# Kernel tuning notes

Measured on AMD Instinct MI355X. Metric: run time of the kernel, lower is better.

The kernel has to match this reference:

```python
import jax, jax.numpy as jnp
import numpy as np

RES = 512
RANK = 48
OUT = 32
N = 1_000_000
INIT = 0.1


def _contract_linf(xyz, aabb):
    # L-infinity cuboid contraction of unbounded coords into [-1,1]^3.
    center = (aabb[:3] + aabb[3:]) * 0.5
    half = jnp.maximum((aabb[3:] - aabb[:3]) * 0.5, 1e-6)
    x = (xyz - center) / half
    linf = jnp.max(jnp.abs(x), axis=-1, keepdims=True)
    safe = jnp.maximum(linf, 1.0)
    scale = jnp.where(linf > 1.0, (2.0 - 1.0 / safe) / safe, 1.0)
    return jnp.clip(x * scale, -1.0, 1.0)


def _sample_plane(plane, gx, gy):
    # plane: [R, Res, Res]; gx,gy in [-1,1] shape [N]; bilinear, align_corners=True.
    res = plane.shape[-1]
    fx = (gx + 1.0) * 0.5 * (res - 1)
    fy = (gy + 1.0) * 0.5 * (res - 1)
    x0 = jnp.clip(jnp.floor(fx), 0, res - 2).astype(jnp.int32)
    y0 = jnp.clip(jnp.floor(fy), 0, res - 2).astype(jnp.int32)
    wx = fx - x0
    wy = fy - y0
    x1 = x0 + 1
    y1 = y0 + 1
    # gathers -> [R, N]
    v = (plane[:, y0, x0] * ((1 - wy) * (1 - wx))
         + plane[:, y0, x1] * ((1 - wy) * wx)
         + plane[:, y1, x0] * (wy * (1 - wx))
         + plane[:, y1, x1] * (wy * wx))
    return v


def _sample_line(line, g):
    # line: [R, Res]; 1-D linear interp along the resolution axis (align_corners=True).
    res = line.shape[-1]
    f = (g + 1.0) * 0.5 * (res - 1)
    i0 = jnp.clip(jnp.floor(f), 0, res - 2).astype(jnp.int32)
    w = f - i0
    return line[:, i0] * (1 - w) + line[:, i0 + 1] * w  # [R, N]


def setup_inputs() -> dict:
    key = jax.random.key(0)
    ks = jax.random.split(key, 9)
    coordinates = jax.random.normal(ks[0], (N, 3), dtype=jnp.float32) * 1.5  # some points outside aabb
    aabb = jnp.array([-1.0, -1.0, -1.0, 1.0, 1.0, 1.0], dtype=jnp.float32)
    plane_xy = jax.random.normal(ks[1], (RANK, RES, RES), dtype=jnp.float32) * INIT
    plane_xz = jax.random.normal(ks[2], (RANK, RES, RES), dtype=jnp.float32) * INIT
    plane_yz = jax.random.normal(ks[3], (RANK, RES, RES), dtype=jnp.float32) * INIT
    line_z = jax.random.normal(ks[4], (RANK, RES), dtype=jnp.float32) * INIT
    line_y = jax.random.normal(ks[5], (RANK, RES), dtype=jnp.float32) * INIT
    line_x = jax.random.normal(ks[6], (RANK, RES), dtype=jnp.float32) * INIT
    W = jax.random.normal(ks[7], (OUT, RANK), dtype=jnp.float32) * INIT
    b = jnp.zeros((OUT,), dtype=jnp.float32)
    return {"coordinates": coordinates, "aabb": aabb,
            "plane_xy": plane_xy, "plane_xz": plane_xz, "plane_yz": plane_yz,
            "line_z": line_z, "line_y": line_y, "line_x": line_x,
            "W": W, "b": b}


def reference(coordinates, aabb, plane_xy, plane_xz, plane_yz, line_z, line_y, line_x, W, b):
    c = _contract_linf(coordinates, aabb)  # [N,3] in [-1,1]
    cx, cy, cz = c[:, 0], c[:, 1], c[:, 2]
    # VM decomposition: plane(a,b) * line(c), summed over the three permutations -> [R, N]
    vm = (_sample_plane(plane_xy, cx, cy) * _sample_line(line_z, cz)
          + _sample_plane(plane_xz, cx, cz) * _sample_line(line_y, cy)
          + _sample_plane(plane_yz, cy, cz) * _sample_line(line_x, cx))
    # projection rank -> out_channels: [N, OUT]
    return jnp.einsum('rn,or->no', vm, W) + b
```

## Files before the change

kernel.cpp:

```cpp
#include <hip/hip_runtime.h>
#include <stdint.h>

#define RES 512
#define RANK 48
#define OUT_CH 32
#define KBITS 5
#define NBKT (1 << (3 * KBITS))
#define STR 32

typedef unsigned int u32;
typedef unsigned short u16;
typedef u32 u32x4 __attribute__((ext_vector_type(4)));


static __device__ __forceinline__ u16 f2bf(float f){
  u32 u = __float_as_uint(f);
  u32 r = (u + 0x7fffu + ((u >> 16) & 1u)) >> 16;
  return (u16)r;
}

static __device__ __forceinline__ void axis_setup(float c, int& o, float& w){
  float f = (c + 1.f) * 255.5f;
  float of = fminf(fmaxf(floorf(f), 0.f), 510.f);
  o = (int)of; w = f - of;
}

static __device__ __forceinline__ void contract(const float* __restrict__ aabb,
                                                float px, float py, float pz,
                                                float& cx, float& cy, float& cz){
  float c0 = (aabb[0] + aabb[3]) * 0.5f;
  float c1 = (aabb[1] + aabb[4]) * 0.5f;
  float c2 = (aabb[2] + aabb[5]) * 0.5f;
  float h0 = fmaxf((aabb[3] - aabb[0]) * 0.5f, 1e-6f);
  float h1 = fmaxf((aabb[4] - aabb[1]) * 0.5f, 1e-6f);
  float h2 = fmaxf((aabb[5] - aabb[2]) * 0.5f, 1e-6f);
  float x0 = (px - c0) / h0;
  float x1 = (py - c1) / h1;
  float x2 = (pz - c2) / h2;
  float linf = fmaxf(fabsf(x0), fmaxf(fabsf(x1), fabsf(x2)));
  float scale = 1.f;
  if (linf > 1.f){ float inv = 1.f / linf; scale = (2.f - inv) * inv; }
  cx = fminf(fmaxf(x0 * scale, -1.f), 1.f);
  cy = fminf(fmaxf(x1 * scale, -1.f), 1.f);
  cz = fminf(fmaxf(x2 * scale, -1.f), 1.f);
}

static __device__ __forceinline__ u32 spread3(u32 x){
  x &= 0x3FF;
  x = (x | (x << 16)) & 0x030000FF;
  x = (x | (x <<  8)) & 0x0300F00F;
  x = (x | (x <<  4)) & 0x030C30C3;
  x = (x | (x <<  2)) & 0x09249249;
  return x;
}

static __device__ __forceinline__ u32 morton_key(float cx, float cy, float cz){
  u32 kx = (u32)fminf(fmaxf((cx + 1.f) * 16.f, 0.f), 31.f);
  u32 ky = (u32)fminf(fmaxf((cy + 1.f) * 16.f, 0.f), 31.f);
  u32 kz = (u32)fminf(fmaxf((cz + 1.f) * 16.f, 0.f), 31.f);
  return spread3(kx) | (spread3(ky) << 1) | (spread3(kz) << 2);
}


__global__ void zero_hist(u32* __restrict__ hist)
{
  hist[blockIdx.x * 1024 + threadIdx.x] = 0u;
}


#define TRANS_P 3072
#define TRANS_L 6

template<bool STAGE>
__global__ void prep_fused(const float* __restrict__ pxy, const float* __restrict__ pxz,
                           const float* __restrict__ pyz,
                           const float* __restrict__ lz, const float* __restrict__ ly,
                           const float* __restrict__ lx,
                           const float* __restrict__ coords, const float* __restrict__ aabb,
                           u32* __restrict__ dstP, u32* __restrict__ dstL,
                           u32* __restrict__ hist, u32* __restrict__ keyrank,
                           float4* __restrict__ staged, int n)
{
  __shared__ u32 lds[256 * 25];
  int bid = blockIdx.x;
  int tid = threadIdx.x;
  if (bid < TRANS_P){
    int xh = bid & 1, y = (bid >> 1) & 511, p = bid >> 10;
    const float* src = (p == 0) ? pxy : (p == 1) ? pxz : pyz;
    int x = xh * 256 + tid;
    #pragma unroll
    for (int r2 = 0; r2 < 24; ++r2){
      float f0 = src[((size_t)(2 * r2) * RES + y) * RES + x];
      float f1 = src[((size_t)(2 * r2 + 1) * RES + y) * RES + x];
      lds[tid * 25 + r2] = (u32)f2bf(f0) | ((u32)f2bf(f1) << 16);
    }
    __syncthreads();
    u32* dplane = dstP + (size_t)p * (RES * RES * STR);
    size_t base = ((size_t)y * RES + xh * 256) * STR;
    for (int t = tid; t < 256 * STR; t += 256){
      int tex = t >> 5, r = t & 31;
      dplane[base + t] = (r < 24) ? lds[tex * 25 + r] : 0u;
    }
  } else if (bid < TRANS_P + TRANS_L){
    int g = (bid - TRANS_P) * 256 + tid;
    if (g < 3 * RES){
      int p = g >> 9, i = g & 511;
      const float* src = (p == 0) ? lz : (p == 1) ? ly : lx;
      u32* d = dstL + (size_t)g * STR;
      #pragma unroll
      for (int r2 = 0; r2 < 24; ++r2){
        float f0 = src[(2 * r2) * RES + i];
        float f1 = src[(2 * r2 + 1) * RES + i];
        d[r2] = (u32)f2bf(f0) | ((u32)f2bf(f1) << 16);
      }
      #pragma unroll
      for (int r2 = 24; r2 < STR; ++r2) d[r2] = 0u;
    }
  } else {
    int i = (bid - TRANS_P - TRANS_L) * 256 + tid;
    if (i < n){
      float cx, cy, cz;
      contract(aabb, coords[3*i], coords[3*i+1], coords[3*i+2], cx, cy, cz);
      u32 key = morton_key(cx, cy, cz);
      u32 rank = atomicAdd(hist + key, 1u);
      keyrank[i] = (rank << 15) | key;
      if (STAGE) staged[i] = make_float4(cx, cy, cz, __uint_as_float((u32)i));
    }
  }
}


__global__ void scan_kernel(u32* __restrict__ hist)
{
  __shared__ u32 part[1024];
  int tid = threadIdx.x;
  int base = tid * 32;
  u32 loc[32];
  u32 s = 0;
  #pragma unroll
  for (int j = 0; j < 32; j++){ loc[j] = hist[base + j]; s += loc[j]; }
  part[tid] = s;
  __syncthreads();
  for (int off = 1; off < 1024; off <<= 1){
    u32 v = 0;
    if (tid >= off) v = part[tid - off];
    __syncthreads();
    part[tid] += v;
    __syncthreads();
  }
  u32 run = part[tid] - s;
  #pragma unroll
  for (int j = 0; j < 32; j++){ u32 t = loc[j]; hist[base + j] = run; run += t; }
}


__global__ void key_scatter_staged(const u32* __restrict__ base, const u32* __restrict__ keyrank,
                                   const float4* __restrict__ staged, float4* __restrict__ sorted, int n)
{
  int i = blockIdx.x * 256 + threadIdx.x;
  if (i >= n) return;
  u32 kr = keyrank[i];
  u32 pos = base[kr & 0x7FFFu] + (kr >> 15);
  sorted[pos] = staged[i];
}


__global__ void key_scatter(const float* __restrict__ coords, const float* __restrict__ aabb,
                            const u32* __restrict__ base, const u32* __restrict__ keyrank,
                            float4* __restrict__ sorted, int n)
{
  int i = blockIdx.x * 256 + threadIdx.x;
  if (i >= n) return;
  float cx, cy, cz;
  contract(aabb, coords[3*i], coords[3*i+1], coords[3*i+2], cx, cy, cz);
  u32 kr = keyrank[i];
  u32 pos = base[kr & 0x7FFFu] + (kr >> 15);
  sorted[pos] = make_float4(cx, cy, cz, __uint_as_float((u32)i));
}


#define EXLO(u) __uint_as_float((u) << 16)
#define EXHI(u) __uint_as_float((u) & 0xffff0000u)

#define CORN_INIT(ps, taddr, wc) \
  { u32x4 _t = *(const u32x4*)(taddr); \
    _Pragma("unroll") for (int c = 0; c < 4; c++){ \
      ps[2*c] = EXLO(_t[c]) * (wc); ps[2*c+1] = EXHI(_t[c]) * (wc); } }

#define CORN_ACC(ps, taddr, wc) \
  { u32x4 _t = *(const u32x4*)(taddr); \
    _Pragma("unroll") for (int c = 0; c < 4; c++){ \
      ps[2*c] = fmaf(EXLO(_t[c]), (wc), ps[2*c]); ps[2*c+1] = fmaf(EXHI(_t[c]), (wc), ps[2*c+1]); } }

template<bool SORTED>
__global__ __launch_bounds__(256, 2)
void geo_coop(const float4* __restrict__ sorted,
              const float* __restrict__ coords, const float* __restrict__ aabb,
              const u32* __restrict__ pl, const u32* __restrict__ ln,
              const float* __restrict__ W, const float* __restrict__ bias,
              float* __restrict__ out, int n, int nwg)
{
  __shared__ __align__(16) float Wlds[8 * 49 * 4];
  __shared__ __align__(16) float vmlds[32][68];

  for (int e = threadIdx.x; e < 8 * RANK * 4; e += 256){
    int k = e / (RANK * 4);
    int rem = e - k * (RANK * 4);
    int r = rem >> 2, j = rem & 3;
    Wlds[(k * 49 + r) * 4 + j] = W[(4 * k + j) * RANK + r];
  }
  __syncthreads();

  int bid = blockIdx.x;
  int swz;
  if (SORTED){
    int q = nwg >> 3, r8 = nwg & 7;
    int xcd = bid & 7, sub = bid >> 3;
    swz = (xcd < r8 ? xcd * (q + 1) : r8 * (q + 1) + (xcd - r8) * q) + sub;
  } else {
    swz = bid;
  }

  int g = threadIdx.x >> 3;
  int k = threadIdx.x & 7;
  int i = swz * 32 + g;
  bool valid = i < n;
  int ic = valid ? i : (n - 1);

  float cx, cy, cz; u32 oidx;
  if (SORTED){
    u32x4 pr = __builtin_nontemporal_load((const u32x4*)(sorted + ic));
    cx = __uint_as_float(pr[0]);
    cy = __uint_as_float(pr[1]);
    cz = __uint_as_float(pr[2]);
    oidx = pr[3];
  } else {
    contract(aabb, coords[3*ic], coords[3*ic+1], coords[3*ic+2], cx, cy, cz);
    oidx = (u32)ic;
  }

  int ox, oy, oz; float wx, wy, wz;
  axis_setup(cx, ox, wx); axis_setup(cy, oy, wy); axis_setup(cz, oz, wz);
  float uxw = 1.f - wx, uyw = 1.f - wy, uzw = 1.f - wz;

  const u32* A   = pl + ((size_t)oy * RES + ox) * STR + 4 * k;
  const u32* B   = pl + (size_t)RES * RES * STR     + ((size_t)oz * RES + ox) * STR + 4 * k;
  const u32* C   = pl + (size_t)2 * RES * RES * STR + ((size_t)oz * RES + oy) * STR + 4 * k;
  const u32* LZp = ln +                          (size_t)oz * STR + 4 * k;
  const u32* LYp = ln + (size_t)RES * STR     + (size_t)oy * STR + 4 * k;
  const u32* LXp = ln + (size_t)2 * RES * STR + (size_t)ox * STR + 4 * k;

  float vm8[8];
  #pragma unroll
  for (int j = 0; j < 8; j++) vm8[j] = 0.f;

  {
    u32x4 l0 = *(const u32x4*)(LZp);
    u32x4 l1 = *(const u32x4*)(LZp + STR);
    float lv8[8], ps8[8];
    #pragma unroll
    for (int c = 0; c < 4; c++){
      float a0 = EXLO(l0[c]), a1 = EXHI(l0[c]);
      float b0 = EXLO(l1[c]), b1 = EXHI(l1[c]);
      lv8[2*c]   = fmaf(wz, b0 - a0, a0);
      lv8[2*c+1] = fmaf(wz, b1 - a1, a1);
    }
    CORN_INIT(ps8, A,                 uyw * uxw);
    CORN_ACC (ps8, A + STR,           uyw * wx);
    CORN_ACC (ps8, A + RES * STR,     wy * uxw);
    CORN_ACC (ps8, A + RES * STR + STR, wy * wx);
    #pragma unroll
    for (int j = 0; j < 8; j++) vm8[j] = fmaf(ps8[j], lv8[j], vm8[j]);
  }
  {
    u32x4 l0 = *(const u32x4*)(LYp);
    u32x4 l1 = *(const u32x4*)(LYp + STR);
    float lv8[8], ps8[8];
    #pragma unroll
    for (int c = 0; c < 4; c++){
      float a0 = EXLO(l0[c]), a1 = EXHI(l0[c]);
      float b0 = EXLO(l1[c]), b1 = EXHI(l1[c]);
      lv8[2*c]   = fmaf(wy, b0 - a0, a0);
      lv8[2*c+1] = fmaf(wy, b1 - a1, a1);
    }
    CORN_INIT(ps8, B,                 uzw * uxw);
    CORN_ACC (ps8, B + STR,           uzw * wx);
    CORN_ACC (ps8, B + RES * STR,     wz * uxw);
    CORN_ACC (ps8, B + RES * STR + STR, wz * wx);
    #pragma unroll
    for (int j = 0; j < 8; j++) vm8[j] = fmaf(ps8[j], lv8[j], vm8[j]);
  }
  {
    u32x4 l0 = *(const u32x4*)(LXp);
    u32x4 l1 = *(const u32x4*)(LXp + STR);
    float lv8[8], ps8[8];
    #pragma unroll
    for (int c = 0; c < 4; c++){
      float a0 = EXLO(l0[c]), a1 = EXHI(l0[c]);
      float b0 = EXLO(l1[c]), b1 = EXHI(l1[c]);
      lv8[2*c]   = fmaf(wx, b0 - a0, a0);
      lv8[2*c+1] = fmaf(wx, b1 - a1, a1);
    }
    CORN_INIT(ps8, C,                 uzw * uyw);
    CORN_ACC (ps8, C + STR,           uzw * wy);
    CORN_ACC (ps8, C + RES * STR,     wz * uyw);
    CORN_ACC (ps8, C + RES * STR + STR, wz * wy);
    #pragma unroll
    for (int j = 0; j < 8; j++) vm8[j] = fmaf(ps8[j], lv8[j], vm8[j]);
  }

  *(float4*)&vmlds[g][8 * k]     = make_float4(vm8[0], vm8[1], vm8[2], vm8[3]);
  *(float4*)&vmlds[g][8 * k + 4] = make_float4(vm8[4], vm8[5], vm8[6], vm8[7]);
  __syncthreads();

  float vmv[RANK];
  #pragma unroll
  for (int qd = 0; qd < 12; qd++){
    float4 v4 = *(const float4*)&vmlds[g][qd * 4];
    vmv[4*qd+0] = v4.x; vmv[4*qd+1] = v4.y; vmv[4*qd+2] = v4.z; vmv[4*qd+3] = v4.w;
  }
  float4 accv = ((const float4*)bias)[k];
  const float4* wk = (const float4*)(Wlds + (size_t)k * 49 * 4);
  #pragma unroll
  for (int r = 0; r < RANK; r++){
    float4 w4 = wk[r];
    accv.x = fmaf(vmv[r], w4.x, accv.x);
    accv.y = fmaf(vmv[r], w4.y, accv.y);
    accv.z = fmaf(vmv[r], w4.z, accv.z);
    accv.w = fmaf(vmv[r], w4.w, accv.w);
  }

  if (valid){
    *(float4*)(out + (size_t)oidx * 32 + 4 * k) = accv;
  }
}


__global__ __launch_bounds__(256, 2)
void geo_direct(const float* __restrict__ coords, const float* __restrict__ aabb,
                const float* __restrict__ PXY, const float* __restrict__ PXZ, const float* __restrict__ PYZ,
                const float* __restrict__ LZ, const float* __restrict__ LY, const float* __restrict__ LX,
                const float* __restrict__ W, const float* __restrict__ bias,
                float* __restrict__ out, int n)
{
  __shared__ __align__(16) float Wt[RANK * OUT_CH];
  for (int t = threadIdx.x; t < RANK * OUT_CH; t += 256){
    int r = t >> 5, o = t & 31;
    Wt[t] = W[o * RANK + r];
  }
  __syncthreads();

  int i = blockIdx.x * 256 + threadIdx.x;
  if (i >= n) return;

  float cx, cy, cz;
  contract(aabb, coords[3*i], coords[3*i+1], coords[3*i+2], cx, cy, cz);
  int ox, oy, oz; float wx, wy, wz;
  axis_setup(cx, ox, wx); axis_setup(cy, oy, wy); axis_setup(cz, oz, wz);

  int offA = oy * RES + ox, offB = oz * RES + ox, offC = oz * RES + oy;
  float uxw = 1.f - wx, uyw = 1.f - wy, uzw = 1.f - wz;
  float aw00 = uyw*uxw, aw01 = uyw*wx, aw10 = wy*uxw, aw11 = wy*wx;
  float bw00 = uzw*uxw, bw01 = uzw*wx, bw10 = wz*uxw, bw11 = wz*wx;
  float cw00 = uzw*uyw, cw01 = uzw*wy, cw10 = wz*uyw, cw11 = wz*wy;

  float acc[OUT_CH];
  #pragma unroll
  for (int o = 0; o < 8; o++){
    float4 bv = *(const float4*)(bias + o * 4);
    acc[4*o+0] = bv.x; acc[4*o+1] = bv.y; acc[4*o+2] = bv.z; acc[4*o+3] = bv.w;
  }
  const float4* Wt4 = (const float4*)Wt;

  for (int r = 0; r < RANK; r++){
    const float* pA = PXY + (size_t)r * RES * RES;
    const float* pB = PXZ + (size_t)r * RES * RES;
    const float* pC = PYZ + (size_t)r * RES * RES;
    float va = fmaf(pA[offA], aw00, fmaf(pA[offA+1], aw01, fmaf(pA[offA+RES], aw10, pA[offA+RES+1]*aw11)));
    float vb = fmaf(pB[offB], bw00, fmaf(pB[offB+1], bw01, fmaf(pB[offB+RES], bw10, pB[offB+RES+1]*bw11)));
    float vc = fmaf(pC[offC], cw00, fmaf(pC[offC+1], cw01, fmaf(pC[offC+RES], cw10, pC[offC+RES+1]*cw11)));
    float l0;
    l0 = LZ[r * RES + oz];
    float lzv = fmaf(wz, LZ[r * RES + oz + 1] - l0, l0);
    l0 = LY[r * RES + oy];
    float lyv = fmaf(wy, LY[r * RES + oy + 1] - l0, l0);
    l0 = LX[r * RES + ox];
    float lxv = fmaf(wx, LX[r * RES + ox + 1] - l0, l0);
    float vm = fmaf(va, lzv, fmaf(vb, lyv, vc * lxv));
    const float4* wrow = Wt4 + r * 8;
    #pragma unroll
    for (int q = 0; q < 8; q++){
      float4 w4 = wrow[q];
      acc[4*q+0] = fmaf(vm, w4.x, acc[4*q+0]); acc[4*q+1] = fmaf(vm, w4.y, acc[4*q+1]);
      acc[4*q+2] = fmaf(vm, w4.z, acc[4*q+2]); acc[4*q+3] = fmaf(vm, w4.w, acc[4*q+3]);
    }
  }

  float4* o4 = (float4*)(out + (size_t)i * 32);
  #pragma unroll
  for (int q = 0; q < 8; q++)
    o4[q] = make_float4(acc[4*q+0], acc[4*q+1], acc[4*q+2], acc[4*q+3]);
}


extern "C" void kernel_launch(void* const* d_in, const int* in_sizes, int n_in,
                              void* d_out, int out_size, void* d_ws, size_t ws_size,
                              hipStream_t stream)
{
  const float* coords = (const float*)d_in[0];
  const float* aabb   = (const float*)d_in[1];
  const float* pxy    = (const float*)d_in[2];
  const float* pxz    = (const float*)d_in[3];
  const float* pyz    = (const float*)d_in[4];
  const float* lz     = (const float*)d_in[5];
  const float* ly     = (const float*)d_in[6];
  const float* lx     = (const float*)d_in[7];
  const float* W      = (const float*)d_in[8];
  const float* bias   = (const float*)d_in[9];
  float* out = (float*)d_out;
  int n = in_sizes[0] / 3;
  int nwg256 = (n + 255) / 256;
  int nwg32  = (n + 31) / 32;

  const size_t planesU = (size_t)3 * RES * RES * STR;
  const size_t linesU  = (size_t)3 * RES * STR;
  const size_t histU   = NBKT;
  const size_t keyrU   = (size_t)n;
  const size_t sortedU = (size_t)4 * n;
  const size_t stagedU = (size_t)4 * n;
  const size_t needStaged = (planesU + linesU + histU + keyrU + sortedU + stagedU) * 4;
  const size_t needFull   = (planesU + linesU + histU + keyrU + sortedU) * 4;

  if (ws_size >= needStaged){
    u32* pl      = (u32*)d_ws;
    u32* ln      = pl + planesU;
    u32* hist    = ln + linesU;
    u32* keyrank = hist + histU;
    float4* sorted = (float4*)(keyrank + keyrU);
    float4* staged = sorted + n;
    zero_hist<<<NBKT / 1024, 1024, 0, stream>>>(hist);
    prep_fused<true><<<TRANS_P + TRANS_L + nwg256, 256, 0, stream>>>(
        pxy, pxz, pyz, lz, ly, lx, coords, aabb, pl, ln, hist, keyrank, staged, n);
    scan_kernel<<<1, 1024, 0, stream>>>(hist);
    key_scatter_staged<<<nwg256, 256, 0, stream>>>(hist, keyrank, staged, sorted, n);
    geo_coop<true><<<nwg32, 256, 0, stream>>>(sorted, nullptr, nullptr, pl, ln, W, bias, out, n, nwg32);
  } else if (ws_size >= needFull){
    u32* pl      = (u32*)d_ws;
    u32* ln      = pl + planesU;
    u32* hist    = ln + linesU;
    u32* keyrank = hist + histU;
    float4* sorted = (float4*)(keyrank + keyrU);
    zero_hist<<<NBKT / 1024, 1024, 0, stream>>>(hist);
    prep_fused<false><<<TRANS_P + TRANS_L + nwg256, 256, 0, stream>>>(
        pxy, pxz, pyz, lz, ly, lx, coords, aabb, pl, ln, hist, keyrank, nullptr, n);
    scan_kernel<<<1, 1024, 0, stream>>>(hist);
    key_scatter<<<nwg256, 256, 0, stream>>>(coords, aabb, hist, keyrank, sorted, n);
    geo_coop<true><<<nwg32, 256, 0, stream>>>(sorted, nullptr, nullptr, pl, ln, W, bias, out, n, nwg32);
  } else if (ws_size >= (planesU + linesU) * 4){
    u32* pl = (u32*)d_ws;
    u32* ln = pl + planesU;
    prep_fused<false><<<TRANS_P + TRANS_L, 256, 0, stream>>>(
        pxy, pxz, pyz, lz, ly, lx, coords, aabb, pl, ln, (u32*)pl, (u32*)pl, nullptr, 0);
    geo_coop<false><<<nwg32, 256, 0, stream>>>(nullptr, coords, aabb, pl, ln, W, bias, out, n, nwg32);
  } else {
    geo_direct<<<nwg256, 256, 0, stream>>>(coords, aabb, pxy, pxz, pyz, lz, ly, lx, W, bias, out, n);
  }
}
```

Before: 340.3 us.

## Split histogram scan across blocks and raise geo_coop occupancy hint

Replaces the single-block 32K-bucket exclusive scan with a two-level scan: 32 blocks each scan 1024 buckets and write block totals, then a tiny kernel scans the totals, and the scatter kernels add the block offset. This spreads the scan over many CUs instead of one workgroup, at the cost of an extra launch and an extra lookup per point in the scatter. It also raises the geo_coop launch_bounds minimum blocks per CU from 2 to 8, which can force register spilling in the main gather kernel.

```diff
diff --git a/kernel.cpp b/kernel.cpp
--- a/kernel.cpp
+++ b/kernel.cpp
@@ -130,51 +130,59 @@
 }
 
 
-__global__ void scan_kernel(u32* __restrict__ hist)
+__global__ void scan_blocks(u32* __restrict__ hist, u32* __restrict__ tops)
 {
   __shared__ u32 part[1024];
   int tid = threadIdx.x;
-  int base = tid * 32;
-  u32 loc[32];
-  u32 s = 0;
-  #pragma unroll
-  for (int j = 0; j < 32; j++){ loc[j] = hist[base + j]; s += loc[j]; }
-  part[tid] = s;
+  int idx = blockIdx.x * 1024 + tid;
+  u32 v = hist[idx];
+  part[tid] = v;
   __syncthreads();
   for (int off = 1; off < 1024; off <<= 1){
-    u32 v = 0;
-    if (tid >= off) v = part[tid - off];
+    u32 t = 0;
+    if (tid >= off) t = part[tid - off];
     __syncthreads();
-    part[tid] += v;
+    part[tid] += t;
     __syncthreads();
   }
-  u32 run = part[tid] - s;
-  #pragma unroll
-  for (int j = 0; j < 32; j++){ u32 t = loc[j]; hist[base + j] = run; run += t; }
-}
-
-
-__global__ void key_scatter_staged(const u32* __restrict__ base, const u32* __restrict__ keyrank,
+  hist[idx] = part[tid] - v;
+  if (tid == 1023) tops[blockIdx.x] = part[tid];
+}
+
+__global__ void scan_tops(u32* __restrict__ tops)
+{
+  if (threadIdx.x == 0 && blockIdx.x == 0){
+    u32 run = 0;
+    #pragma unroll
+    for (int b = 0; b < NBKT / 1024; b++){ u32 t = tops[b]; tops[b] = run; run += t; }
+  }
+}
+
+
+__global__ void key_scatter_staged(const u32* __restrict__ hist, const u32* __restrict__ tops,
+                                   const u32* __restrict__ keyrank,
                                    const float4* __restrict__ staged, float4* __restrict__ sorted, int n)
 {
   int i = blockIdx.x * 256 + threadIdx.x;
   if (i >= n) return;
   u32 kr = keyrank[i];
-  u32 pos = base[kr & 0x7FFFu] + (kr >> 15);
+  u32 key = kr & 0x7FFFu;
+  u32 pos = tops[key >> 10] + hist[key] + (kr >> 15);
   sorted[pos] = staged[i];
 }
 
 
 __global__ void key_scatter(const float* __restrict__ coords, const float* __restrict__ aabb,
-                            const u32* __restrict__ base, const u32* __restrict__ keyrank,
-                            float4* __restrict__ sorted, int n)
+                            const u32* __restrict__ hist, const u32* __restrict__ tops,
+                            const u32* __restrict__ keyrank, float4* __restrict__ sorted, int n)
 {
   int i = blockIdx.x * 256 + threadIdx.x;
   if (i >= n) return;
   float cx, cy, cz;
   contract(aabb, coords[3*i], coords[3*i+1], coords[3*i+2], cx, cy, cz);
   u32 kr = keyrank[i];
-  u32 pos = base[kr & 0x7FFFu] + (kr >> 15);
+  u32 key = kr & 0x7FFFu;
+  u32 pos = tops[key >> 10] + hist[key] + (kr >> 15);
   sorted[pos] = make_float4(cx, cy, cz, __uint_as_float((u32)i));
 }
 
@@ -193,7 +201,7 @@
       ps[2*c] = fmaf(EXLO(_t[c]), (wc), ps[2*c]); ps[2*c+1] = fmaf(EXHI(_t[c]), (wc), ps[2*c+1]); } }
 
 template<bool SORTED>
-__global__ __launch_bounds__(256, 2)
+__global__ __launch_bounds__(256, 8)
 void geo_coop(const float4* __restrict__ sorted,
               const float* __restrict__ coords, const float* __restrict__ aabb,
               const u32* __restrict__ pl, const u32* __restrict__ ln,
@@ -425,36 +433,41 @@
   const size_t planesU = (size_t)3 * RES * RES * STR;
   const size_t linesU  = (size_t)3 * RES * STR;
   const size_t histU   = NBKT;
+  const size_t topsU   = 64;
   const size_t keyrU   = (size_t)n;
   const size_t sortedU = (size_t)4 * n;
   const size_t stagedU = (size_t)4 * n;
-  const size_t needStaged = (planesU + linesU + histU + keyrU + sortedU + stagedU) * 4;
-  const size_t needFull   = (planesU + linesU + histU + keyrU + sortedU) * 4;
+  const size_t needStaged = (planesU + linesU + histU + topsU + keyrU + sortedU + stagedU) * 4;
+  const size_t needFull   = (planesU + linesU + histU + topsU + keyrU + sortedU) * 4;
 
   if (ws_size >= needStaged){
     u32* pl      = (u32*)d_ws;
     u32* ln      = pl + planesU;
     u32* hist    = ln + linesU;
-    u32* keyrank = hist + histU;
+    u32* tops    = hist + histU;
+    u32* keyrank = tops + topsU;
     float4* sorted = (float4*)(keyrank + keyrU);
     float4* staged = sorted + n;
     zero_hist<<<NBKT / 1024, 1024, 0, stream>>>(hist);
     prep_fused<true><<<TRANS_P + TRANS_L + nwg256, 256, 0, stream>>>(
         pxy, pxz, pyz, lz, ly, lx, coords, aabb, pl, ln, hist, keyrank, staged, n);
-    scan_kernel<<<1, 1024, 0, stream>>>(hist);
-    key_scatter_staged<<<nwg256, 256, 0, stream>>>(hist, keyrank, staged, sorted, n);
+    scan_blocks<<<NBKT / 1024, 1024, 0, stream>>>(hist, tops);
+    scan_tops<<<1, 64, 0, stream>>>(tops);
+    key_scatter_staged<<<nwg256, 256, 0, stream>>>(hist, tops, keyrank, staged, sorted, n);
     geo_coop<true><<<nwg32, 256, 0, stream>>>(sorted, nullptr, nullptr, pl, ln, W, bias, out, n, nwg32);
   } else if (ws_size >= needFull){
     u32* pl      = (u32*)d_ws;
     u32* ln      = pl + planesU;
     u32* hist    = ln + linesU;
-    u32* keyrank = hist + histU;
+    u32* tops    = hist + histU;
+    u32* keyrank = tops + topsU;
     float4* sorted = (float4*)(keyrank + keyrU);
     zero_hist<<<NBKT / 1024, 1024, 0, stream>>>(hist);
     prep_fused<false><<<TRANS_P + TRANS_L + nwg256, 256, 0, stream>>>(
         pxy, pxz, pyz, lz, ly, lx, coords, aabb, pl, ln, hist, keyrank, nullptr, n);
-    scan_kernel<<<1, 1024, 0, stream>>>(hist);
-    key_scatter<<<nwg256, 256, 0, stream>>>(coords, aabb, hist, keyrank, sorted, n);
+    scan_blocks<<<NBKT / 1024, 1024, 0, stream>>>(hist, tops);
+    scan_tops<<<1, 64, 0, stream>>>(tops);
+    key_scatter<<<nwg256, 256, 0, stream>>>(coords, aabb, hist, tops, keyrank, sorted, n);
     geo_coop<true><<<nwg32, 256, 0, stream>>>(sorted, nullptr, nullptr, pl, ln, W, bias, out, n, nwg32);
   } else if (ws_size >= (planesU + linesU) * 4){
     u32* pl = (u32*)d_ws;
```

Result: slower. 905.8 us (+166.2%).
